# Kernel optimization log

Hardware: AMD Instinct MI355X
Metric: run time of the kernel (lower is better)

The kernel has to match this reference:

```python
import jax, jax.numpy as jnp
import numpy as np

N = 50000   # nodes
E = 500000  # edges
S = 64      # 0e channels in node feats
V = 32      # 1o channels in node feats
R = 32      # radial/scalar edge features
MLPW = 128
AVG = 10.0  # avg_num_neighbors
SQ3 = np.float32(np.sqrt(3.0))
SQ2 = np.float32(np.sqrt(2.0))


def setup_inputs() -> dict:
    key = jax.random.key(0)
    ks = jax.random.split(key, 10)
    node_scalars = jax.random.normal(ks[0], (N, S), jnp.float32)
    node_vectors = jax.random.normal(ks[1], (N, V, 3), jnp.float32)
    ev = jax.random.normal(ks[2], (E, 3), jnp.float32)
    # l=1 spherical harmonics of unit edge vectors, component normalization (|Y1| = sqrt(3))
    edge_vec = ev / jnp.linalg.norm(ev, axis=1, keepdims=True) * SQ3
    scalar_edge_feats = jax.random.normal(ks[3], (E, R), jnp.float32)
    lengths = jax.random.uniform(ks[4], (E, 1), jnp.float32)
    senders = jax.random.randint(ks[5], (E,), 0, N, jnp.int32)
    receivers = jax.random.randint(ks[6], (E,), 0, N, jnp.int32)
    din = 2 * S + R + 1  # 161
    num_irreps = V + (S + V)  # 128 gate scalars
    def lin(k, i, o):
        return jax.random.normal(k, (i, o), jnp.float32) / np.float32(np.sqrt(i))
    return {
        "node_scalars": node_scalars, "node_vectors": node_vectors,
        "edge_vec": edge_vec, "scalar_edge_feats": scalar_edge_feats,
        "lengths": lengths, "senders": senders, "receivers": receivers,
        "W1": lin(ks[7], din, MLPW), "b1": jnp.zeros((MLPW,), jnp.float32),
        "W2": lin(ks[8], MLPW, MLPW), "b2": jnp.zeros((MLPW,), jnp.float32),
        "W3": lin(ks[9], MLPW, num_irreps), "b3": jnp.zeros((num_irreps,), jnp.float32),
    }


def reference(node_scalars, node_vectors, edge_vec, scalar_edge_feats, lengths,
              senders, receivers, W1, b1, W2, b2, W3, b3):
    # gather sender features
    s_snd = node_scalars[senders]          # [E, S]
    v_snd = node_vectors[senders]          # [E, V, 3]
    # Clebsch-Gordan tensor product with 1o edge harmonics (component normalization):
    m0 = jnp.einsum('eca,ea->ec', v_snd, edge_vec) / SQ3          # 1o x 1o -> 0e, [E, V]
    m1a = s_snd[:, :, None] * edge_vec[:, None, :]                 # 0e x 1o -> 1o, [E, S, 3]
    m1b = jnp.cross(v_snd, edge_vec[:, None, :]) / SQ2             # 1o x 1o -> 1o, [E, V, 3]
    # MLP gate on concatenated scalars
    mlp_in = jnp.concatenate([s_snd, node_scalars[receivers], scalar_edge_feats, lengths], axis=1)
    h = jax.nn.silu(mlp_in @ W1 + b1)
    h = jax.nn.silu(h @ W2 + b2)
    mix = h @ W3 + b3                                               # [E, V + S + V]
    m0 = m0 * mix[:, :V]
    m1 = jnp.concatenate([m1a, m1b], axis=1) * mix[:, V:, None]     # [E, S+V, 3]
    # scatter-add to receivers
    out0 = jax.ops.segment_sum(m0, receivers, num_segments=N)      # [N, V]
    out1 = jax.ops.segment_sum(m1, receivers, num_segments=N)      # [N, S+V, 3]
    return jnp.concatenate([out0, out1.reshape(N, -1)], axis=1) / AVG
```

## Files before the change

kernel.cpp:

```cpp
#include <hip/hip_runtime.h>

#define N_NODES 50000
#define N_EDGES 500000
#define EB 64
#define HST 136
#define W1K 176
#define OUTC 320
#define MROW 208
#define NBLK1 49
#define KP1 200
#define KH  136
#define KV  104
#define WTS 40
#define INV_SQ3 0.57735026918962576f
#define INV_SQ2 0.70710678118654752f
#define INV_AVG 0.1f

typedef short bf16x8 __attribute__((ext_vector_type(8)));
typedef unsigned short u16;
typedef u16 u16x8 __attribute__((ext_vector_type(8)));
typedef float f32x16 __attribute__((ext_vector_type(16)));

__device__ __forceinline__ unsigned cvtpk(float lo, float hi) {
    unsigned r;
    asm("v_cvt_pk_bf16_f32 %0, %1, %2" : "=v"(r) : "v"(lo), "v"(hi));
    return r;
}
__device__ __forceinline__ u16 f2bf(float f) { return (u16)cvtpk(f, f); }
__device__ __forceinline__ float bf2f(u16 h) {
    union { unsigned u; float f; } x; x.u = ((unsigned)h) << 16; return x.f;
}
__device__ __forceinline__ float fsilu(float x) {
    return x * __builtin_amdgcn_rcpf(1.f + __expf(-x));
}

__device__ __forceinline__ void stage16(const float* g, u16* l, bool v) {
    float4 a0, a1, a2, a3;
    const float4 z = make_float4(0.f, 0.f, 0.f, 0.f);
    if (v) { a0 = *(const float4*)(g);     a1 = *(const float4*)(g + 4);
             a2 = *(const float4*)(g + 8); a3 = *(const float4*)(g + 12); }
    else   { a0 = z; a1 = z; a2 = z; a3 = z; }
    uint4 p0 = { cvtpk(a0.x, a0.y), cvtpk(a0.z, a0.w), cvtpk(a1.x, a1.y), cvtpk(a1.z, a1.w) };
    uint4 p1 = { cvtpk(a2.x, a2.y), cvtpk(a2.z, a2.w), cvtpk(a3.x, a3.y), cvtpk(a3.z, a3.w) };
    *(uint4*)(l) = p0; *(uint4*)(l + 8) = p1;
}
__device__ __forceinline__ void stage8(const float* g, u16* l, bool v) {
    float4 a0, a1;
    const float4 z = make_float4(0.f, 0.f, 0.f, 0.f);
    if (v) { a0 = *(const float4*)(g); a1 = *(const float4*)(g + 4); }
    else   { a0 = z; a1 = z; }
    uint4 p0 = { cvtpk(a0.x, a0.y), cvtpk(a0.z, a0.w), cvtpk(a1.x, a1.y), cvtpk(a1.z, a1.w) };
    *(uint4*)(l) = p0;
}


__global__ void hist_kernel(const int* __restrict__ recv, int* __restrict__ counts) {
    const int e = blockIdx.x * 256 + threadIdx.x;
    if (e < N_EDGES) atomicAdd(&counts[recv[e]], 1);
}

__global__ __launch_bounds__(256) void scan_k1(const int* __restrict__ counts,
                                               int* __restrict__ rowp,
                                               int* __restrict__ partials) {
    __shared__ int sd[256];
    const int t = threadIdx.x;
    const int base = blockIdx.x * 1024 + t * 4;
    int c0 = 0, c1 = 0, c2 = 0, c3 = 0;
    if (base + 3 < N_NODES) {
        int4 v = *(const int4*)&counts[base];
        c0 = v.x; c1 = v.y; c2 = v.z; c3 = v.w;
    } else {
        if (base     < N_NODES) c0 = counts[base];
        if (base + 1 < N_NODES) c1 = counts[base + 1];
        if (base + 2 < N_NODES) c2 = counts[base + 2];
        if (base + 3 < N_NODES) c3 = counts[base + 3];
    }
    const int T = c0 + c1 + c2 + c3;
    sd[t] = T; __syncthreads();
    for (int off = 1; off < 256; off <<= 1) {
        int v = (t >= off) ? sd[t - off] : 0;
        __syncthreads();
        sd[t] += v;
        __syncthreads();
    }
    const int excl = sd[t] - T;
    if (base     < N_NODES) rowp[base]     = excl;
    if (base + 1 < N_NODES) rowp[base + 1] = excl + c0;
    if (base + 2 < N_NODES) rowp[base + 2] = excl + c0 + c1;
    if (base + 3 < N_NODES) rowp[base + 3] = excl + c0 + c1 + c2;
    if (t == 255) partials[blockIdx.x] = sd[255];
}

__global__ __launch_bounds__(64) void scan_k2(int* __restrict__ partials) {
    __shared__ int sd[64];
    const int t = threadIdx.x;
    const int v0 = (t < NBLK1) ? partials[t] : 0;
    sd[t] = v0; __syncthreads();
    for (int off = 1; off < 64; off <<= 1) {
        int v = (t >= off) ? sd[t - off] : 0;
        __syncthreads();
        sd[t] += v;
        __syncthreads();
    }
    if (t < NBLK1) partials[t] = sd[t] - v0;
}

__global__ __launch_bounds__(256) void scan_k3(int* __restrict__ rowp,
                                               const int* __restrict__ partials,
                                               int* __restrict__ cursors) {
    const int add = partials[blockIdx.x];
    const int base = blockIdx.x * 1024 + threadIdx.x * 4;
    #pragma unroll
    for (int i = 0; i < 4; ++i) {
        const int idx = base + i;
        if (idx < N_NODES) {
            const int v = rowp[idx] + add;
            rowp[idx] = v;
            cursors[idx] = v;
        }
    }
    if (blockIdx.x == 0 && threadIdx.x == 0) rowp[N_NODES] = N_EDGES;
}

__global__ void fill_kernel(const int* __restrict__ recv,
                            const int* __restrict__ snd,
                            int* __restrict__ cursors,
                            int* __restrict__ elist,
                            int* __restrict__ esnd,
                            int* __restrict__ ercv) {
    const int e = blockIdx.x * 256 + threadIdx.x;
    if (e < N_EDGES) {
        const int r = recv[e];
        const int pos = atomicAdd(&cursors[r], 1);
        elist[pos] = e;
        esnd[pos]  = snd[e];
        ercv[pos]  = r;
    }
}


#define WT_TOTAL (128 * W1K + 2 * 128 * 128)

__global__ __launch_bounds__(256)
void wcvt_kernel(const float* __restrict__ W1, const float* __restrict__ W2,
                 const float* __restrict__ W3, u16* __restrict__ wt) {
    const int i = blockIdx.x * 256 + threadIdx.x;
    if (i < 128 * W1K) {
        const int n = i / W1K, k = i - n * W1K;
        wt[i] = (k < 161) ? f2bf(W1[(size_t)k * 128 + n]) : (u16)0;
    } else if (i < 128 * W1K + 128 * 128) {
        const int j = i - 128 * W1K;
        const int n = j >> 7, k = j & 127;
        wt[i] = f2bf(W2[(size_t)k * 128 + n]);
    } else if (i < WT_TOTAL) {
        const int j = i - 128 * W1K - 128 * 128;
        const int n = j >> 7, k = j & 127;
        wt[i] = f2bf(W3[(size_t)k * 128 + n]);
    }
}


#define NS_ELEMS (N_NODES * 64)
#define NV_ELEMS (N_NODES * 96)

__global__ __launch_bounds__(256)
void nodecvt_kernel(const float* __restrict__ ns, const float* __restrict__ nv,
                    u16* __restrict__ nsb, u16* __restrict__ nvb) {
    const int i2 = (blockIdx.x * 256 + threadIdx.x) * 2;
    if (i2 < NS_ELEMS) {
        float2 v = *(const float2*)(ns + i2);
        *(unsigned*)(nsb + i2) = cvtpk(v.x, v.y);
    } else if (i2 < NS_ELEMS + NV_ELEMS) {
        const int j2 = i2 - NS_ELEMS;
        float2 v = *(const float2*)(nv + j2);
        *(unsigned*)(nvb + j2) = cvtpk(v.x, v.y);
    }
}


__global__ __launch_bounds__(256)
void edgeperm_kernel(const int* __restrict__ elist,
                     const float* __restrict__ sef,
                     const float* __restrict__ len,
                     const float* __restrict__ ev,
                     u16* __restrict__ sefp,
                     u16* __restrict__ lenp,
                     float* __restrict__ evp) {
    const int s2 = blockIdx.x * 256 + threadIdx.x;
    const int slot = s2 >> 1, h = s2 & 1;
    if (slot >= N_EDGES) return;
    const int e = elist[slot];
    const float* src = sef + (size_t)e * 32 + h * 16;
    u16* dst = sefp + (size_t)slot * 32 + h * 16;
    float4 a0 = ((const float4*)src)[0], a1 = ((const float4*)src)[1];
    float4 a2 = ((const float4*)src)[2], a3 = ((const float4*)src)[3];
    uint4 p0 = { cvtpk(a0.x, a0.y), cvtpk(a0.z, a0.w), cvtpk(a1.x, a1.y), cvtpk(a1.z, a1.w) };
    uint4 p1 = { cvtpk(a2.x, a2.y), cvtpk(a2.z, a2.w), cvtpk(a3.x, a3.y), cvtpk(a3.z, a3.w) };
    ((uint4*)dst)[0] = p0; ((uint4*)dst)[1] = p1;
    if (h == 0) {
        lenp[slot] = f2bf(len[e]);
        const float* ep = ev + (size_t)e * 3;
        float* dp = evp + (size_t)slot * 3;
        dp[0] = ep[0]; dp[1] = ep[1]; dp[2] = ep[2];
    }
}


__global__ __launch_bounds__(256, 5)
void mlp_msg_kernel(const u16* __restrict__ ns_bf,
                    const u16* __restrict__ nv_bf,
                    const int* __restrict__ esnd,
                    const int* __restrict__ ercv,
                    const u16* __restrict__ sefp,
                    const u16* __restrict__ lenp,
                    const float* __restrict__ evp,
                    const u16* __restrict__ wt,
                    const float* __restrict__ b1,
                    const float* __restrict__ b2,
                    const float* __restrict__ b3,
                    u16* __restrict__ msg, int slo, int cnt)
{
    __shared__ u16 Hb[EB * HST];

    const int t = threadIdx.x;
    const int lbase = blockIdx.x * EB;
    const int w = t >> 6, l = t & 63;
    const int lr = l & 31, lg = l >> 5;
    const int m0 = (w >> 1) * 32, n0 = (w & 1) * 64;

    const int lsA   = lbase + m0 + lr;
    const int slotA = slo + (lsA < cnt ? lsA : 0);
    const int siA = esnd[slotA];
    const int riA = ercv[slotA];

    const int me = t >> 2, q = t & 3;
    const int lsE = lbase + me;
    const bool veE = lsE < cnt;
    const int slotE = slo + (veE ? lsE : 0);
    const int siE = esnd[slotE];
    const float evx = evp[(size_t)slotE * 3 + 0];
    const float evy = evp[(size_t)slotE * 3 + 1];
    const float evz = evp[(size_t)slotE * 3 + 2];

    bf16x8 afr[11];
    {
        const u16* sp = ns_bf + (size_t)siA * 64 + lg * 8;
        const u16* rp = ns_bf + (size_t)riA * 64 + lg * 8;
        const u16* fp = sefp + (size_t)slotA * 32 + lg * 8;
        #pragma unroll
        for (int ks = 0; ks < 4; ++ks) afr[ks]     = *(const bf16x8*)(sp + ks * 16);
        #pragma unroll
        for (int ks = 0; ks < 4; ++ks) afr[4 + ks] = *(const bf16x8*)(rp + ks * 16);
        afr[8] = *(const bf16x8*)(fp);
        afr[9] = *(const bf16x8*)(fp + 16);
        bf16x8 z = (bf16x8)0;
        if (lg == 0) z[0] = (short)lenp[slotA];
        afr[10] = z;
    }

    const u16* w1t = wt;
    const u16* w2t = wt + 128 * W1K;
    const u16* w3t = w2t + 128 * 128;

    f32x16 acc0, acc1;

    #pragma unroll
    for (int i = 0; i < 16; ++i) { acc0[i] = 0.f; acc1[i] = 0.f; }
    {
        const u16* bp0 = w1t + (size_t)(n0 + lr) * W1K + lg * 8;
        const u16* bp1 = bp0 + 32 * W1K;
        #pragma unroll
        for (int ks = 0; ks < 11; ++ks) {
            bf16x8 bv0 = *(const bf16x8*)(bp0 + ks * 16);
            bf16x8 bv1 = *(const bf16x8*)(bp1 + ks * 16);
            acc0 = __builtin_amdgcn_mfma_f32_32x32x16_bf16(afr[ks], bv0, acc0, 0, 0, 0);
            acc1 = __builtin_amdgcn_mfma_f32_32x32x16_bf16(afr[ks], bv1, acc1, 0, 0, 0);
        }
    }
    {   const float bv0 = b1[n0 + lr], bv1 = b1[n0 + 32 + lr];
        #pragma unroll
        for (int r = 0; r < 16; ++r) {
            const int row = (r & 3) + 8 * (r >> 2) + 4 * lg;
            Hb[(m0 + row) * HST + n0 + lr]      = f2bf(fsilu(acc0[r] + bv0));
            Hb[(m0 + row) * HST + n0 + 32 + lr] = f2bf(fsilu(acc1[r] + bv1));
        }
    }
    __syncthreads();

    auto run_layer_lds = [&](const u16* Wg, f32x16& a0, f32x16& a1) {
        #pragma unroll
        for (int i = 0; i < 16; ++i) { a0[i] = 0.f; a1[i] = 0.f; }
        const u16* ap  = Hb + (m0 + lr) * HST + lg * 8;
        const u16* bp0 = Wg + (size_t)(n0 + lr) * 128 + lg * 8;
        const u16* bp1 = bp0 + 32 * 128;
        #pragma unroll
        for (int ks = 0; ks < 8; ++ks) {
            bf16x8 af  = *(const bf16x8*)(ap  + ks * 16);
            bf16x8 bv0 = *(const bf16x8*)(bp0 + ks * 16);
            bf16x8 bv1 = *(const bf16x8*)(bp1 + ks * 16);
            a0 = __builtin_amdgcn_mfma_f32_32x32x16_bf16(af, bv0, a0, 0, 0, 0);
            a1 = __builtin_amdgcn_mfma_f32_32x32x16_bf16(af, bv1, a1, 0, 0, 0);
        }
    };

    run_layer_lds(w2t, acc0, acc1);
    __syncthreads();
    {   const float bv0 = b2[n0 + lr], bv1 = b2[n0 + 32 + lr];
        #pragma unroll
        for (int r = 0; r < 16; ++r) {
            const int row = (r & 3) + 8 * (r >> 2) + 4 * lg;
            Hb[(m0 + row) * HST + n0 + lr]      = f2bf(fsilu(acc0[r] + bv0));
            Hb[(m0 + row) * HST + n0 + 32 + lr] = f2bf(fsilu(acc1[r] + bv1));
        }
    }
    __syncthreads();

    run_layer_lds(w3t, acc0, acc1);
    __syncthreads();
    {   const float bv0 = b3[n0 + lr], bv1 = b3[n0 + 32 + lr];
        #pragma unroll
        for (int r = 0; r < 16; ++r) {
            const int row = (r & 3) + 8 * (r >> 2) + 4 * lg;
            Hb[(m0 + row) * HST + n0 + lr]      = f2bf(acc0[r] + bv0);
            Hb[(m0 + row) * HST + n0 + 32 + lr] = f2bf(acc1[r] + bv1);
        }
    }
    __syncthreads();

    if (veE) {
        const u16* Hr = Hb + me * HST;
        u16* mrow = msg + (size_t)lsE * MROW;

        u16 sa[16], va[24];
        {
            const u16* nsrow = ns_bf + (size_t)siE * 64 + 16 * q;
            *(u16x8*)(sa)     = *(const u16x8*)(nsrow);
            *(u16x8*)(sa + 8) = *(const u16x8*)(nsrow + 8);
            const u16* nvrow = nv_bf + (size_t)siE * 96 + 24 * q;
            *(u16x8*)(va)      = *(const u16x8*)(nvrow);
            *(u16x8*)(va + 8)  = *(const u16x8*)(nvrow + 8);
            *(u16x8*)(va + 16) = *(const u16x8*)(nvrow + 16);
        }

        float m0v[8], m1bv[24];
        #pragma unroll
        for (int j = 0; j < 8; ++j) {
            const int c = 8 * q + j;
            const float vx = bf2f(va[3 * j]), vy = bf2f(va[3 * j + 1]), vz = bf2f(va[3 * j + 2]);
            m0v[j] = (vx * evx + vy * evy + vz * evz) * INV_SQ3 * bf2f(Hr[c]);
            const float gb = bf2f(Hr[96 + c]) * INV_SQ2;
            m1bv[3 * j + 0] = (vy * evz - vz * evy) * gb;
            m1bv[3 * j + 1] = (vz * evx - vx * evz) * gb;
            m1bv[3 * j + 2] = (vx * evy - vy * evx) * gb;
        }
        {   uint4 o = { cvtpk(m0v[0], m0v[1]), cvtpk(m0v[2], m0v[3]),
                        cvtpk(m0v[4], m0v[5]), cvtpk(m0v[6], m0v[7]) };
            *(uint4*)(mrow + 8 * q) = o;
        }
        {   u16* dst = mrow + 96 + 24 * q;
            uint4 o0 = { cvtpk(m1bv[0],  m1bv[1]),  cvtpk(m1bv[2],  m1bv[3]),
                         cvtpk(m1bv[4],  m1bv[5]),  cvtpk(m1bv[6],  m1bv[7])  };
            uint4 o1 = { cvtpk(m1bv[8],  m1bv[9]),  cvtpk(m1bv[10], m1bv[11]),
                         cvtpk(m1bv[12], m1bv[13]), cvtpk(m1bv[14], m1bv[15]) };
            uint4 o2 = { cvtpk(m1bv[16], m1bv[17]), cvtpk(m1bv[18], m1bv[19]),
                         cvtpk(m1bv[20], m1bv[21]), cvtpk(m1bv[22], m1bv[23]) };
            *(uint4*)(dst)      = o0;
            *(uint4*)(dst + 8)  = o1;
            *(uint4*)(dst + 16) = o2;
        }
        {   float sg[16];
            #pragma unroll
            for (int j = 0; j < 16; ++j) {
                const int k = 16 * q + j;
                sg[j] = bf2f(sa[j]) * bf2f(Hr[32 + k]);
            }
            u16* dst = mrow + 32 + 16 * q;
            uint4 o0 = { cvtpk(sg[0],  sg[1]),  cvtpk(sg[2],  sg[3]),
                         cvtpk(sg[4],  sg[5]),  cvtpk(sg[6],  sg[7])  };
            uint4 o1 = { cvtpk(sg[8],  sg[9]),  cvtpk(sg[10], sg[11]),
                         cvtpk(sg[12], sg[13]), cvtpk(sg[14], sg[15]) };
            *(uint4*)(dst)     = o0;
            *(uint4*)(dst + 8) = o1;
        }
        if (q == 0) {
            uint4 e4 = { __builtin_bit_cast(unsigned, evx),
                         __builtin_bit_cast(unsigned, evy),
                         __builtin_bit_cast(unsigned, evz), 0u };
            *(uint4*)(mrow + 192) = e4;
            uint4 z4 = { 0u, 0u, 0u, 0u };
            *(uint4*)(mrow + 200) = z4;
        }
    }
}


__global__ __launch_bounds__(256)
void msg_gather_seq(const int* __restrict__ rowp,
                    const u16* __restrict__ msg,
                    float* __restrict__ out,
                    int slo, int shi, int first)
{
    __shared__ float oacc[4][OUTC];

    const int gw = (blockIdx.x * 256 + threadIdx.x) >> 6;
    const int l  = threadIdx.x & 63;
    const bool nvalid = gw < N_NODES;

    const int rp0 = nvalid ? rowp[gw] : 0;
    const int rp1 = nvalid ? rowp[gw + 1] : 0;
    const int lo = rp0 > slo ? rp0 : slo;
    const int hi = rp1 < shi ? rp1 : shi;
    const int n  = hi > lo ? hi - lo : 0;

    const int half = (l >= 26) ? 1 : 0;
    const int sl   = l - 26 * half;
    const bool lact = (l < 52) && (sl < 24);
    const int seg  = (sl < 4) ? 0 : (sl < 12 ? 1 : 2);

    float acc[24];
    #pragma unroll
    for (int i = 0; i < 24; ++i) acc[i] = 0.f;

    const u16* mb = msg + (size_t)(lo - slo) * MROW;

    auto body = [&](int row) {
        const u16* rp = mb + (size_t)row * MROW + sl * 8;
        const u16x8 v = *(const u16x8*)rp;
        if (seg == 1) {
            const float4 e4 = *(const float4*)(mb + (size_t)row * MROW + 192);
            #pragma unroll
            for (int i = 0; i < 8; ++i) {
                const float s = bf2f(v[i]);
                acc[3 * i + 0] += s * e4.x;
                acc[3 * i + 1] += s * e4.y;
                acc[3 * i + 2] += s * e4.z;
            }
        } else {
            #pragma unroll
            for (int i = 0; i < 8; ++i) acc[i] += bf2f(v[i]);
        }
    };

    int j = 0;
    for (; j + 4 <= n; j += 4) {
        if (lact) { body(j + half); body(j + 2 + half); }
    }
    for (; j + 2 <= n; j += 2) {
        if (lact) body(j + half);
    }
    if (j < n && half == 0 && lact) body(j);

    float* oa = oacc[(threadIdx.x >> 6)];

    if (half == 0 && lact) {
        if (seg == 0) {
            #pragma unroll
            for (int i = 0; i < 8; ++i) oa[sl * 8 + i] = acc[i];
        } else if (seg == 1) {
            const int k0 = (sl - 4) * 8;
            #pragma unroll
            for (int i = 0; i < 8; ++i) {
                oa[32 + 3 * (k0 + i) + 0] = acc[3 * i + 0];
                oa[32 + 3 * (k0 + i) + 1] = acc[3 * i + 1];
                oa[32 + 3 * (k0 + i) + 2] = acc[3 * i + 2];
            }
        } else {
            const int c0 = (sl - 12) * 8;
            #pragma unroll
            for (int i = 0; i < 8; ++i) oa[224 + c0 + i] = acc[i];
        }
    }
    __syncthreads();
    if (half == 1 && lact) {
        if (seg == 0) {
            #pragma unroll
            for (int i = 0; i < 8; ++i) oa[sl * 8 + i] += acc[i];
        } else if (seg == 1) {
            const int k0 = (sl - 4) * 8;
            #pragma unroll
            for (int i = 0; i < 8; ++i) {
                oa[32 + 3 * (k0 + i) + 0] += acc[3 * i + 0];
                oa[32 + 3 * (k0 + i) + 1] += acc[3 * i + 1];
                oa[32 + 3 * (k0 + i) + 2] += acc[3 * i + 2];
            }
        } else {
            const int c0 = (sl - 12) * 8;
            #pragma unroll
            for (int i = 0; i < 8; ++i) oa[224 + c0 + i] += acc[i];
        }
    }
    __syncthreads();

    if (nvalid && l < 40) {
        float r[8];
        #pragma unroll
        for (int i = 0; i < 8; ++i) r[i] = oa[l * 8 + i] * INV_AVG;
        float* orow = out + (size_t)gw * OUTC + l * 8;
        if (first) {
            *(float4*)(orow)     = make_float4(r[0], r[1], r[2], r[3]);
            *(float4*)(orow + 4) = make_float4(r[4], r[5], r[6], r[7]);
        } else if (n > 0) {
            float4 p0 = *(const float4*)(orow);
            float4 p1 = *(const float4*)(orow + 4);
            p0.x += r[0]; p0.y += r[1]; p0.z += r[2]; p0.w += r[3];
            p1.x += r[4]; p1.y += r[5]; p1.z += r[6]; p1.w += r[7];
            *(float4*)(orow)     = p0;
            *(float4*)(orow + 4) = p1;
        }
    }
}


__global__ __launch_bounds__(256, 2)
void fused_mpconv_atomic(const float* __restrict__ node_scalars,
                         const float* __restrict__ node_vectors,
                         const float* __restrict__ edge_vec,
                         const float* __restrict__ sef,
                         const float* __restrict__ lengths,
                         const int* __restrict__ senders,
                         const int* __restrict__ receivers,
                         const float* __restrict__ W1, const float* __restrict__ b1,
                         const float* __restrict__ W2, const float* __restrict__ b2,
                         const float* __restrict__ W3, const float* __restrict__ b3,
                         float* __restrict__ out)
{
    __shared__ u16 A [EB * KP1];
    __shared__ u16 VS[EB * KV];
    __shared__ u16 Hb[EB * KH];
    __shared__ u16 Wt[2][128 * WTS];
    __shared__ float evl[3][EB];
    __shared__ int sidx[EB], ridx[EB];

    const int t = threadIdx.x;
    const int ebase = blockIdx.x * EB;

    {   const int e = t & 63, sub = t >> 6;
        const int eg = ebase + e; const bool ve = eg < N_EDGES;
        if (sub == 0)      sidx[e] = ve ? senders[eg] : 0;
        else if (sub == 1) ridx[e] = ve ? receivers[eg] : 0;
        else if (sub == 2) {
            evl[0][e] = ve ? edge_vec[(size_t)eg * 3 + 0] : 0.f;
            evl[1][e] = ve ? edge_vec[(size_t)eg * 3 + 1] : 0.f;
            evl[2][e] = ve ? edge_vec[(size_t)eg * 3 + 2] : 0.f;
        }
    }
    __syncthreads();

    {   const int me = t >> 2, q = t & 3;
        const int eg = ebase + me; const bool ve = eg < N_EDGES;
        const int si = sidx[me], ri = ridx[me];
        u16* Ar = A + me * KP1;
        stage16(node_scalars + (size_t)si * 64 + q * 16, Ar + q * 16,       ve);
        stage16(node_scalars + (size_t)ri * 64 + q * 16, Ar + 64 + q * 16,  ve);
        stage8 (sef          + (size_t)eg * 32 + q * 8,  Ar + 128 + q * 8,  ve);
        u16x8 zz = (u16x8)0;
        *(u16x8*)(Ar + 160 + q * 8) = zz;
        if (q == 0) *(u16x8*)(Ar + 192) = zz;
        stage16(node_vectors + (size_t)si * 96 + q * 24,      VS + me * KV + q * 24,      ve);
        stage8 (node_vectors + (size_t)si * 96 + q * 24 + 16, VS + me * KV + q * 24 + 16, ve);
        if (q == 0) Ar[160] = f2bf(ve ? lengths[eg] : 0.f);
    }
    __syncthreads();

    const int w  = t >> 6, l = t & 63;
    const int lr = l & 31;
    const int lg = l >> 5;
    const int m0 = (w >> 1) * 32;
    const int n0 = (w & 1) * 64;

    f32x16 acc0, acc1;
    const int n  = t & 127, ph = t >> 7;

    auto run_layer = [&](const u16* Asrc, int astr, const float* Wg, int Kr, int nsteps,
                         f32x16& a0, f32x16& a1) {
        #pragma unroll
        for (int i = 0; i < 16; ++i) { a0[i] = 0.f; a1[i] = 0.f; }
        #pragma unroll
        for (int i = 0; i < 4; ++i) {
            int kl = (i * 2 + ph) * 2;
            float v0 = (kl     < Kr) ? Wg[(size_t)kl * 128 + n]       : 0.f;
            float v1 = (kl + 1 < Kr) ? Wg[(size_t)(kl + 1) * 128 + n] : 0.f;
            *(unsigned*)&Wt[0][n * WTS + kl] = cvtpk(v0, v1);
        }
        __syncthreads();
        const u16* ap = Asrc + (m0 + lr) * astr + lg * 8;
        for (int ks = 0; ks < nsteps; ++ks) {
            const int cur = ks & 1;
            float v0[4], v1[4];
            const int kb = (ks + 1) * 16;
            if (ks + 1 < nsteps) {
                #pragma unroll
                for (int i = 0; i < 4; ++i) {
                    int kg = kb + (i * 2 + ph) * 2;
                    v0[i] = (kg     < Kr) ? Wg[(size_t)kg * 128 + n]       : 0.f;
                    v1[i] = (kg + 1 < Kr) ? Wg[(size_t)(kg + 1) * 128 + n] : 0.f;
                }
            }
            bf16x8 af = *(const bf16x8*)(ap + ks * 16);
            bf16x8 bf0 = *(const bf16x8*)(&Wt[cur][(n0      + lr) * WTS + lg * 8]);
            bf16x8 bf1 = *(const bf16x8*)(&Wt[cur][(n0 + 32 + lr) * WTS + lg * 8]);
            a0 = __builtin_amdgcn_mfma_f32_32x32x16_bf16(af, bf0, a0, 0, 0, 0);
            a1 = __builtin_amdgcn_mfma_f32_32x32x16_bf16(af, bf1, a1, 0, 0, 0);
            if (ks + 1 < nsteps) {
                #pragma unroll
                for (int i = 0; i < 4; ++i) {
                    int kl = (i * 2 + ph) * 2;
                    *(unsigned*)&Wt[cur ^ 1][n * WTS + kl] = cvtpk(v0[i], v1[i]);
                }
            }
            __syncthreads();
        }
    };

    run_layer(A, KP1, W1, 161, 11, acc0, acc1);
    {   const float bv0 = b1[n0 + lr], bv1 = b1[n0 + 32 + lr];
        #pragma unroll
        for (int r = 0; r < 16; ++r) {
            const int row = (r & 3) + 8 * (r >> 2) + 4 * lg;
            Hb[(m0 + row) * KH + n0 + lr]      = f2bf(fsilu(acc0[r] + bv0));
            Hb[(m0 + row) * KH + n0 + 32 + lr] = f2bf(fsilu(acc1[r] + bv1));
        }
    }
    __syncthreads();

    run_layer(Hb, KH, W2, 128, 8, acc0, acc1);
    __syncthreads();
    {   const float bv0 = b2[n0 + lr], bv1 = b2[n0 + 32 + lr];
        #pragma unroll
        for (int r = 0; r < 16; ++r) {
            const int row = (r & 3) + 8 * (r >> 2) + 4 * lg;
            Hb[(m0 + row) * KH + n0 + lr]      = f2bf(fsilu(acc0[r] + bv0));
            Hb[(m0 + row) * KH + n0 + 32 + lr] = f2bf(fsilu(acc1[r] + bv1));
        }
    }
    __syncthreads();

    run_layer(Hb, KH, W3, 128, 8, acc0, acc1);
    __syncthreads();
    {   const float bv0 = b3[n0 + lr], bv1 = b3[n0 + 32 + lr];
        #pragma unroll
        for (int r = 0; r < 16; ++r) {
            const int row = (r & 3) + 8 * (r >> 2) + 4 * lg;
            Hb[(m0 + row) * KH + n0 + lr]      = f2bf(acc0[r] + bv0);
            Hb[(m0 + row) * KH + n0 + 32 + lr] = f2bf(acc1[r] + bv1);
        }
    }
    __syncthreads();

    {   const int me = t >> 2, r = t & 3;
        const int eg2 = ebase + me;
        if (eg2 < N_EDGES) {
            const int row = ridx[me];
            const float evx = evl[0][me], evy = evl[1][me], evz = evl[2][me];
            float* orow = out + (size_t)row * OUTC;
            const u16* Ar = A  + me * KP1;
            const u16* Vr = VS + me * KV;
            const u16* Hr = Hb + me * KH;
            for (int col = r; col < OUTC; col += 4) {
                float val;
                if (col < 32) {
                    const int c = col;
                    const float vx = bf2f(Vr[3 * c]), vy = bf2f(Vr[3 * c + 1]), vz = bf2f(Vr[3 * c + 2]);
                    val = (vx * evx + vy * evy + vz * evz) * INV_SQ3 * bf2f(Hr[c]);
                } else {
                    const int idx = col - 32;
                    const int k = idx / 3;
                    const int d = idx - 3 * k;
                    const float g = bf2f(Hr[32 + k]);
                    if (k < 64) {
                        const float evd = (d == 0) ? evx : ((d == 1) ? evy : evz);
                        val = bf2f(Ar[k]) * evd * g;
                    } else {
                        const int c = k - 64;
                        const float vx = bf2f(Vr[3 * c]), vy = bf2f(Vr[3 * c + 1]), vz = bf2f(Vr[3 * c + 2]);
                        float cr;
                        if (d == 0)      cr = vy * evz - vz * evy;
                        else if (d == 1) cr = vz * evx - vx * evz;
                        else             cr = vx * evy - vy * evx;
                        val = cr * INV_SQ2 * g;
                    }
                }
                atomicAdd(&orow[col], val * INV_AVG);
            }
        }
    }
}


extern "C" void kernel_launch(void* const* d_in, const int* in_sizes, int n_in,
                              void* d_out, int out_size, void* d_ws, size_t ws_size,
                              hipStream_t stream) {
    (void)in_sizes; (void)n_in;
    const float* node_scalars = (const float*)d_in[0];
    const float* node_vectors = (const float*)d_in[1];
    const float* edge_vec     = (const float*)d_in[2];
    const float* sef          = (const float*)d_in[3];
    const float* lengths      = (const float*)d_in[4];
    const int*   senders      = (const int*)d_in[5];
    const int*   receivers    = (const int*)d_in[6];
    const float* W1 = (const float*)d_in[7];
    const float* b1 = (const float*)d_in[8];
    const float* W2 = (const float*)d_in[9];
    const float* b2 = (const float*)d_in[10];
    const float* W3 = (const float*)d_in[11];
    const float* b3 = (const float*)d_in[12];
    float* out = (float*)d_out;

    auto align256 = [](size_t x) { return (x + 255) & ~(size_t)255; };

    size_t off = 0;
    const size_t o_counts  = off; off += align256((size_t)N_NODES * sizeof(int));
    const size_t o_rowp    = off; off += align256((size_t)(N_NODES + 1) * sizeof(int));
    const size_t o_cursors = off; off += align256((size_t)(N_NODES + 1) * sizeof(int));
    const size_t o_part    = off; off += align256(64 * sizeof(int));
    const size_t o_elist   = off; off += align256((size_t)N_EDGES * sizeof(int));
    const size_t o_esnd    = off; off += align256((size_t)N_EDGES * sizeof(int));
    const size_t o_ercv    = off; off += align256((size_t)N_EDGES * sizeof(int));
    const size_t o_wt      = off; off += align256((size_t)WT_TOTAL * sizeof(u16));
    const size_t o_nsb     = off; off += align256((size_t)NS_ELEMS * sizeof(u16));
    const size_t o_nvb     = off; off += align256((size_t)NV_ELEMS * sizeof(u16));
    const size_t o_sefp    = off; off += align256((size_t)N_EDGES * 32 * sizeof(u16));
    const size_t o_lenp    = off; off += align256((size_t)N_EDGES * sizeof(u16));
    const size_t o_evp     = off; off += align256((size_t)N_EDGES * 3 * sizeof(float));
    const size_t o_msg     = off;
    const size_t fixed_bytes = off;

    const size_t ROWB = (size_t)MROW * sizeof(u16);
    long Ec = 0;
    if (ws_size > fixed_bytes + (size_t)128 * ROWB) {
        size_t cap_rows = (ws_size - fixed_bytes) / ROWB;
        Ec = ((long)cap_rows - 64) / 64 * 64;
        if (Ec > N_EDGES) Ec = N_EDGES;
    }

    char* ws = (char*)d_ws;

    if (Ec >= 64) {
        int* counts  = (int*)(ws + o_counts);
        int* rowp    = (int*)(ws + o_rowp);
        int* cursors = (int*)(ws + o_cursors);
        int* part    = (int*)(ws + o_part);
        int* elist   = (int*)(ws + o_elist);
        int* esnd    = (int*)(ws + o_esnd);
        int* ercv    = (int*)(ws + o_ercv);
        u16* wt      = (u16*)(ws + o_wt);
        u16* nsb     = (u16*)(ws + o_nsb);
        u16* nvb     = (u16*)(ws + o_nvb);
        u16* sefp    = (u16*)(ws + o_sefp);
        u16* lenp    = (u16*)(ws + o_lenp);
        float* evp   = (float*)(ws + o_evp);
        u16* msg     = (u16*)(ws + o_msg);

        hipMemsetAsync(counts, 0, (size_t)N_NODES * sizeof(int), stream);
        hist_kernel<<<(N_EDGES + 255) / 256, 256, 0, stream>>>(receivers, counts);
        scan_k1<<<NBLK1, 256, 0, stream>>>(counts, rowp, part);
        scan_k2<<<1, 64, 0, stream>>>(part);
        scan_k3<<<NBLK1, 256, 0, stream>>>(rowp, part, cursors);
        fill_kernel<<<(N_EDGES + 255) / 256, 256, 0, stream>>>(
            receivers, senders, cursors, elist, esnd, ercv);
        edgeperm_kernel<<<(N_EDGES * 2 + 255) / 256, 256, 0, stream>>>(
            elist, sef, lengths, edge_vec, sefp, lenp, evp);
        wcvt_kernel<<<(WT_TOTAL + 255) / 256, 256, 0, stream>>>(W1, W2, W3, wt);
        nodecvt_kernel<<<((NS_ELEMS + NV_ELEMS) / 2 + 255) / 256, 256, 0, stream>>>(
            node_scalars, node_vectors, nsb, nvb);

        const int nchunks = (int)((N_EDGES + Ec - 1) / Ec);
        const int ggrid = (N_NODES * 64 + 255) / 256;
        for (int c = 0; c < nchunks; ++c) {
            const int slo = (int)(c * Ec);
            const int cnt = (int)((N_EDGES - slo < Ec) ? (N_EDGES - slo) : Ec);
            mlp_msg_kernel<<<(cnt + EB - 1) / EB, 256, 0, stream>>>(
                nsb, nvb, esnd, ercv, sefp, lenp, evp,
                wt, b1, b2, b3, msg, slo, cnt);
            msg_gather_seq<<<ggrid, 256, 0, stream>>>(
                rowp, msg, out, slo, slo + cnt, c == 0 ? 1 : 0);
        }
    } else {
        hipMemsetAsync(out, 0, (size_t)out_size * sizeof(float), stream);
        fused_mpconv_atomic<<<(N_EDGES + EB - 1) / EB, 256, 0, stream>>>(
            node_scalars, node_vectors, edge_vec, sef, lengths,
            senders, receivers, W1, b1, W2, b2, W3, b3, out);
    }
}
```

Measured before the change: 461.7 us.

## Fuse edge permutation into fill, store messages piece-major, raise occupancy

Edge features are now permuted and converted to bf16 inside fill_kernel, which removes the separate edgeperm kernel and the elist array. The message buffer changes from row-major 208-element rows to 25 planes of 16-byte pieces (piece-major), so the gather kernel reads contiguous rows for each piece and the padding piece goes away. The MLP kernel's launch-bounds occupancy hint rises from 5 to 7 blocks, and the edge-vector loads move later to reduce register pressure. The fused fill now writes scattered 64-byte outputs from uncoalesced atomic positions, and the higher occupancy target may force register spills.

```diff
diff --git a/kernel.cpp b/kernel.cpp
--- a/kernel.cpp
+++ b/kernel.cpp
@@ -6,7 +6,7 @@
 #define HST 136
 #define W1K 176
 #define OUTC 320
-#define MROW 208
+#define NPIECE 25
 #define NBLK1 49
 #define KP1 200
 #define KH  136
@@ -124,17 +124,33 @@
 
 __global__ void fill_kernel(const int* __restrict__ recv,
                             const int* __restrict__ snd,
+                            const float* __restrict__ sef,
+                            const float* __restrict__ ev,
+                            const float* __restrict__ len,
                             int* __restrict__ cursors,
-                            int* __restrict__ elist,
                             int* __restrict__ esnd,
-                            int* __restrict__ ercv) {
+                            int* __restrict__ ercv,
+                            u16* __restrict__ sefp,
+                            u16* __restrict__ lenp,
+                            float* __restrict__ evp) {
     const int e = blockIdx.x * 256 + threadIdx.x;
-    if (e < N_EDGES) {
-        const int r = recv[e];
-        const int pos = atomicAdd(&cursors[r], 1);
-        elist[pos] = e;
-        esnd[pos]  = snd[e];
-        ercv[pos]  = r;
+    if (e >= N_EDGES) return;
+    const int r = recv[e];
+    const int pos = atomicAdd(&cursors[r], 1);
+    esnd[pos] = snd[e];
+    ercv[pos] = r;
+    lenp[pos] = f2bf(len[e]);
+    const float* ep = ev + (size_t)e * 3;
+    float* dp = evp + (size_t)pos * 3;
+    dp[0] = ep[0]; dp[1] = ep[1]; dp[2] = ep[2];
+    const float* sp = sef + (size_t)e * 32;
+    u16* op = sefp + (size_t)pos * 32;
+    #pragma unroll
+    for (int i = 0; i < 4; ++i) {
+        float4 a = ((const float4*)sp)[2 * i];
+        float4 b = ((const float4*)sp)[2 * i + 1];
+        uint4 p = { cvtpk(a.x, a.y), cvtpk(a.z, a.w), cvtpk(b.x, b.y), cvtpk(b.z, b.w) };
+        ((uint4*)op)[i] = p;
     }
 }
 
@@ -178,47 +194,19 @@
 }
 
 
-__global__ __launch_bounds__(256)
-void edgeperm_kernel(const int* __restrict__ elist,
-                     const float* __restrict__ sef,
-                     const float* __restrict__ len,
-                     const float* __restrict__ ev,
-                     u16* __restrict__ sefp,
-                     u16* __restrict__ lenp,
-                     float* __restrict__ evp) {
-    const int s2 = blockIdx.x * 256 + threadIdx.x;
-    const int slot = s2 >> 1, h = s2 & 1;
-    if (slot >= N_EDGES) return;
-    const int e = elist[slot];
-    const float* src = sef + (size_t)e * 32 + h * 16;
-    u16* dst = sefp + (size_t)slot * 32 + h * 16;
-    float4 a0 = ((const float4*)src)[0], a1 = ((const float4*)src)[1];
-    float4 a2 = ((const float4*)src)[2], a3 = ((const float4*)src)[3];
-    uint4 p0 = { cvtpk(a0.x, a0.y), cvtpk(a0.z, a0.w), cvtpk(a1.x, a1.y), cvtpk(a1.z, a1.w) };
-    uint4 p1 = { cvtpk(a2.x, a2.y), cvtpk(a2.z, a2.w), cvtpk(a3.x, a3.y), cvtpk(a3.z, a3.w) };
-    ((uint4*)dst)[0] = p0; ((uint4*)dst)[1] = p1;
-    if (h == 0) {
-        lenp[slot] = f2bf(len[e]);
-        const float* ep = ev + (size_t)e * 3;
-        float* dp = evp + (size_t)slot * 3;
-        dp[0] = ep[0]; dp[1] = ep[1]; dp[2] = ep[2];
-    }
-}
-
-
-__global__ __launch_bounds__(256, 5)
+__global__ __launch_bounds__(256, 7)
 void mlp_msg_kernel(const u16* __restrict__ ns_bf,
                     const u16* __restrict__ nv_bf,
-                    const int* __restrict__ esnd,
-                    const int* __restrict__ ercv,
                     const u16* __restrict__ sefp,
                     const u16* __restrict__ lenp,
                     const float* __restrict__ evp,
+                    const int* __restrict__ esnd,
+                    const int* __restrict__ ercv,
                     const u16* __restrict__ wt,
                     const float* __restrict__ b1,
                     const float* __restrict__ b2,
                     const float* __restrict__ b3,
-                    u16* __restrict__ msg, int slo, int cnt)
+                    u16* __restrict__ msg, long cap, int slo, int cnt)
 {
     __shared__ u16 Hb[EB * HST];
 
@@ -228,19 +216,17 @@
     const int lr = l & 31, lg = l >> 5;
     const int m0 = (w >> 1) * 32, n0 = (w & 1) * 64;
 
-    const int lsA   = lbase + m0 + lr;
-    const int slotA = slo + (lsA < cnt ? lsA : 0);
+    const int lsA   = (lbase + m0 + lr < cnt) ? (lbase + m0 + lr) : (cnt - 1);
+    const int slotA = slo + lsA;
     const int siA = esnd[slotA];
     const int riA = ercv[slotA];
 
     const int me = t >> 2, q = t & 3;
-    const int lsE = lbase + me;
-    const bool veE = lsE < cnt;
-    const int slotE = slo + (veE ? lsE : 0);
+    const int lsE0 = lbase + me;
+    const bool veE = lsE0 < cnt;
+    const int lsE = veE ? lsE0 : (cnt - 1);
+    const int slotE = slo + lsE;
     const int siE = esnd[slotE];
-    const float evx = evp[(size_t)slotE * 3 + 0];
-    const float evy = evp[(size_t)slotE * 3 + 1];
-    const float evz = evp[(size_t)slotE * 3 + 2];
 
     bf16x8 afr[11];
     {
@@ -329,7 +315,11 @@
 
     if (veE) {
         const u16* Hr = Hb + me * HST;
-        u16* mrow = msg + (size_t)lsE * MROW;
+        const float evx = evp[(size_t)slotE * 3 + 0];
+        const float evy = evp[(size_t)slotE * 3 + 1];
+        const float evz = evp[(size_t)slotE * 3 + 2];
+
+        auto pp = [&](int p) { return msg + ((size_t)p * cap + lsE) * 8; };
 
         u16 sa[16], va[24];
         {
@@ -355,18 +345,17 @@
         }
         {   uint4 o = { cvtpk(m0v[0], m0v[1]), cvtpk(m0v[2], m0v[3]),
                         cvtpk(m0v[4], m0v[5]), cvtpk(m0v[6], m0v[7]) };
-            *(uint4*)(mrow + 8 * q) = o;
-        }
-        {   u16* dst = mrow + 96 + 24 * q;
-            uint4 o0 = { cvtpk(m1bv[0],  m1bv[1]),  cvtpk(m1bv[2],  m1bv[3]),
+            *(uint4*)pp(q) = o;
+        }
+        {   uint4 o0 = { cvtpk(m1bv[0],  m1bv[1]),  cvtpk(m1bv[2],  m1bv[3]),
                          cvtpk(m1bv[4],  m1bv[5]),  cvtpk(m1bv[6],  m1bv[7])  };
             uint4 o1 = { cvtpk(m1bv[8],  m1bv[9]),  cvtpk(m1bv[10], m1bv[11]),
                          cvtpk(m1bv[12], m1bv[13]), cvtpk(m1bv[14], m1bv[15]) };
             uint4 o2 = { cvtpk(m1bv[16], m1bv[17]), cvtpk(m1bv[18], m1bv[19]),
                          cvtpk(m1bv[20], m1bv[21]), cvtpk(m1bv[22], m1bv[23]) };
-            *(uint4*)(dst)      = o0;
-            *(uint4*)(dst + 8)  = o1;
-            *(uint4*)(dst + 16) = o2;
+            *(uint4*)pp(12 + 3 * q) = o0;
+            *(uint4*)pp(13 + 3 * q) = o1;
+            *(uint4*)pp(14 + 3 * q) = o2;
         }
         {   float sg[16];
             #pragma unroll
@@ -374,21 +363,18 @@
                 const int k = 16 * q + j;
                 sg[j] = bf2f(sa[j]) * bf2f(Hr[32 + k]);
             }
-            u16* dst = mrow + 32 + 16 * q;
             uint4 o0 = { cvtpk(sg[0],  sg[1]),  cvtpk(sg[2],  sg[3]),
                          cvtpk(sg[4],  sg[5]),  cvtpk(sg[6],  sg[7])  };
             uint4 o1 = { cvtpk(sg[8],  sg[9]),  cvtpk(sg[10], sg[11]),
                          cvtpk(sg[12], sg[13]), cvtpk(sg[14], sg[15]) };
-            *(uint4*)(dst)     = o0;
-            *(uint4*)(dst + 8) = o1;
+            *(uint4*)pp(4 + 2 * q) = o0;
+            *(uint4*)pp(5 + 2 * q) = o1;
         }
         if (q == 0) {
             uint4 e4 = { __builtin_bit_cast(unsigned, evx),
                          __builtin_bit_cast(unsigned, evy),
                          __builtin_bit_cast(unsigned, evz), 0u };
-            *(uint4*)(mrow + 192) = e4;
-            uint4 z4 = { 0u, 0u, 0u, 0u };
-            *(uint4*)(mrow + 200) = z4;
+            *(uint4*)pp(24) = e4;
         }
     }
 }
@@ -396,7 +382,7 @@
 
 __global__ __launch_bounds__(256)
 void msg_gather_seq(const int* __restrict__ rowp,
-                    const u16* __restrict__ msg,
+                    const u16* __restrict__ msg, long cap,
                     float* __restrict__ out,
                     int slo, int shi, int first)
 {
@@ -421,13 +407,14 @@
     #pragma unroll
     for (int i = 0; i < 24; ++i) acc[i] = 0.f;
 
-    const u16* mb = msg + (size_t)(lo - slo) * MROW;
+    const long r0 = lo - slo;
+    const u16* pbase  = msg + ((size_t)sl * cap + r0) * 8;
+    const u16* evbase = msg + ((size_t)24 * cap + r0) * 8;
 
     auto body = [&](int row) {
-        const u16* rp = mb + (size_t)row * MROW + sl * 8;
-        const u16x8 v = *(const u16x8*)rp;
+        const u16x8 v = *(const u16x8*)(pbase + (size_t)row * 8);
         if (seg == 1) {
-            const float4 e4 = *(const float4*)(mb + (size_t)row * MROW + 192);
+            const float4 e4 = *(const float4*)(evbase + (size_t)row * 8);
             #pragma unroll
             for (int i = 0; i < 8; ++i) {
                 const float s = bf2f(v[i]);
@@ -713,7 +700,6 @@
     const size_t o_rowp    = off; off += align256((size_t)(N_NODES + 1) * sizeof(int));
     const size_t o_cursors = off; off += align256((size_t)(N_NODES + 1) * sizeof(int));
     const size_t o_part    = off; off += align256(64 * sizeof(int));
-    const size_t o_elist   = off; off += align256((size_t)N_EDGES * sizeof(int));
     const size_t o_esnd    = off; off += align256((size_t)N_EDGES * sizeof(int));
     const size_t o_ercv    = off; off += align256((size_t)N_EDGES * sizeof(int));
     const size_t o_wt      = off; off += align256((size_t)WT_TOTAL * sizeof(u16));
@@ -725,7 +711,7 @@
     const size_t o_msg     = off;
     const size_t fixed_bytes = off;
 
-    const size_t ROWB = (size_t)MROW * sizeof(u16);
+    const size_t ROWB = (size_t)NPIECE * 16;
     long Ec = 0;
     if (ws_size > fixed_bytes + (size_t)128 * ROWB) {
         size_t cap_rows = (ws_size - fixed_bytes) / ROWB;
@@ -740,7 +726,6 @@
         int* rowp    = (int*)(ws + o_rowp);
         int* cursors = (int*)(ws + o_cursors);
         int* part    = (int*)(ws + o_part);
-        int* elist   = (int*)(ws + o_elist);
         int* esnd    = (int*)(ws + o_esnd);
         int* ercv    = (int*)(ws + o_ercv);
         u16* wt      = (u16*)(ws + o_wt);
@@ -757,12 +742,14 @@
         scan_k2<<<1, 64, 0, stream>>>(part);
         scan_k3<<<NBLK1, 256, 0, stream>>>(rowp, part, cursors);
         fill_kernel<<<(N_EDGES + 255) / 256, 256, 0, stream>>>(
-            receivers, senders, cursors, elist, esnd, ercv);
-        edgeperm_kernel<<<(N_EDGES * 2 + 255) / 256, 256, 0, stream>>>(
-            elist, sef, lengths, edge_vec, sefp, lenp, evp);
+            receivers, senders, sef, edge_vec, lengths,
+            cursors, esnd, ercv, sefp, lenp, evp);
         wcvt_kernel<<<(WT_TOTAL + 255) / 256, 256, 0, stream>>>(W1, W2, W3, wt);
-        nodecvt_kernel<<<((NS_ELEMS + NV_ELEMS) / 2 + 255) / 256, 256, 0, stream>>>(
-            node_scalars, node_vectors, nsb, nvb);
+        {
+            const int tot2 = (NS_ELEMS + NV_ELEMS) / 2;
+            nodecvt_kernel<<<(tot2 + 255) / 256, 256, 0, stream>>>(
+                node_scalars, node_vectors, nsb, nvb);
+        }
 
         const int nchunks = (int)((N_EDGES + Ec - 1) / Ec);
         const int ggrid = (N_NODES * 64 + 255) / 256;
@@ -770,10 +757,10 @@
             const int slo = (int)(c * Ec);
             const int cnt = (int)((N_EDGES - slo < Ec) ? (N_EDGES - slo) : Ec);
             mlp_msg_kernel<<<(cnt + EB - 1) / EB, 256, 0, stream>>>(
-                nsb, nvb, esnd, ercv, sefp, lenp, evp,
-                wt, b1, b2, b3, msg, slo, cnt);
+                nsb, nvb, sefp, lenp, evp, esnd, ercv,
+                wt, b1, b2, b3, msg, Ec, slo, cnt);
             msg_gather_seq<<<ggrid, 256, 0, stream>>>(
-                rowp, msg, out, slo, slo + cnt, c == 0 ? 1 : 0);
+                rowp, msg, Ec, out, slo, slo + cnt, c == 0 ? 1 : 0);
         }
     } else {
         hipMemsetAsync(out, 0, (size_t)out_size * sizeof(float), stream);
```

Result: slower. 497.1 us (+7.7%).
